# Performance work log

Measured on AMD Instinct MI355X. Metric: run time of the kernel, lower is better.

## Reference

```python
import jax, jax.numpy as jnp
import numpy as np
import math

D_MODEL = 1024
NHEAD = 16
K_DIM = D_MODEL // NHEAD
B, S = 2, 2048

def setup_inputs() -> dict:
    key = jax.random.key(0)
    ks = jax.random.split(key, 12)
    sc = 1.0 / math.sqrt(D_MODEL)
    inp = {
        'query': jax.random.normal(ks[0], (B, S, D_MODEL), jnp.float32),
        'key':   jax.random.normal(ks[1], (B, S, D_MODEL), jnp.float32),
        'value': jax.random.normal(ks[2], (B, S, D_MODEL), jnp.float32),
        'Wq': jax.random.normal(ks[3], (D_MODEL, D_MODEL), jnp.float32) * sc,
        'bq': jnp.zeros((D_MODEL,), jnp.float32),
        'Wk': jax.random.normal(ks[4], (D_MODEL, D_MODEL), jnp.float32) * sc,
        'bk': jnp.zeros((D_MODEL,), jnp.float32),
        'Wv': jax.random.normal(ks[5], (D_MODEL, D_MODEL), jnp.float32) * sc,
        'bv': jnp.zeros((D_MODEL,), jnp.float32),
        'Wo': jax.random.normal(ks[6], (D_MODEL, D_MODEL), jnp.float32) * sc,
        'bo': jnp.zeros((D_MODEL,), jnp.float32),
    }
    return inp

def reference(query, key, value, Wq, bq, Wk, bk, Wv, bv, Wo, bo):
    b, s, _ = query.shape
    # Linear projections (torch Linear: x @ W.T + b), split into heads -> [b, h, s, d]
    Q = (query @ Wq.T + bq).reshape(b, s, NHEAD, K_DIM).transpose(0, 2, 1, 3)
    K = (key   @ Wk.T + bk).reshape(b, s, NHEAD, K_DIM).transpose(0, 2, 1, 3)
    V = (value @ Wv.T + bv).reshape(b, s, NHEAD, K_DIM).transpose(0, 2, 1, 3)
    scores = jnp.einsum('bhqd,bhkd->bhqk', Q, K) / math.sqrt(K_DIM)
    attn = jax.nn.softmax(scores, axis=-1)  # dropout = identity (eval)
    out = jnp.einsum('bhqk,bhkd->bhqd', attn, V)
    out = out.transpose(0, 2, 1, 3).reshape(b, s, D_MODEL)
    out = out @ Wo.T + bo
    return (out, attn)
```

## Files before the change

kernel.cpp:

```cpp
#include <hip/hip_runtime.h>
#include <hip/hip_bf16.h>
#include <stdint.h>

#define S_LEN 2048
#define NB 2
#define NH 16
#define DM 1024
#define KDIM 64
#define MTOK (NB*S_LEN)

typedef __attribute__((ext_vector_type(8))) short bf16x8;
typedef __attribute__((ext_vector_type(4))) float f32x4;
typedef __attribute__((ext_vector_type(4))) unsigned short u16x4;
typedef __attribute__((ext_vector_type(8))) unsigned short u16x8;

#define AS1 __attribute__((address_space(1)))
#define AS3 __attribute__((address_space(3)))

__device__ __forceinline__ unsigned short f2bf(float f) {
  unsigned int u = __builtin_bit_cast(unsigned int, f);
  return (unsigned short)((u + 0x7fffu + ((u >> 16) & 1u)) >> 16);
}
__device__ __forceinline__ f32x4 mfma16(bf16x8 a, bf16x8 b, f32x4 c) {
  return __builtin_amdgcn_mfma_f32_16x16x32_bf16(a, b, c, 0, 0, 0);
}

struct CvtArgs {
  const float* src[7];
  unsigned short* dst[7];
  int n[7];
};

__global__ __launch_bounds__(256) void cvt_f32_bf16(CvtArgs a) {
  const int seg = blockIdx.y;
  const float* __restrict__ s = a.src[seg];
  unsigned short* __restrict__ d = a.dst[seg];
  const int n4 = a.n[seg] >> 2;
  const int stride = gridDim.x * blockDim.x;
  for (int i = blockIdx.x * blockDim.x + threadIdx.x; i < n4; i += stride) {
    const float4 v = reinterpret_cast<const float4*>(s)[i];
    u16x4 o;
    o[0] = f2bf(v.x); o[1] = f2bf(v.y); o[2] = f2bf(v.z); o[3] = f2bf(v.w);
    reinterpret_cast<u16x4*>(d)[i] = o;
  }
}

struct GemmArgs {
  const unsigned short* A[3];
  const unsigned short* W[3];
  const float* bias[3];
  void* dst[3];
  int mode[3];
};

__global__ __launch_bounds__(256, 2)
void gemm_pipe(GemmArgs ga)
{
  __shared__ __align__(16) char smem[32768];

  const int z = blockIdx.z;
  const unsigned short* __restrict__ A  = ga.A[z];
  const unsigned short* __restrict__ Bw = ga.W[z];
  const float* __restrict__ bias = ga.bias[z];
  void* __restrict__ dst = ga.dst[z];
  const int mode = ga.mode[z];

  const int t = threadIdx.x;
  const int w = t >> 6, l = t & 63;
  const int g = l >> 4, cl = l & 15;

  const int L   = blockIdx.x + 8 * blockIdx.y;
  const int xcd = L & 7, ix = L >> 3;
  const int m0  = (xcd * 4 + (ix & 3)) * 128;
  const int n0  = (ix >> 2) * 128;

  const unsigned short* Ag = A  + (size_t)(m0 + (t >> 2)) * DM + (t & 3) * 8;
  const unsigned short* Bg = Bw + (size_t)(n0 + (t >> 2)) * DM + (t & 3) * 8;

  const int wm = (w >> 1) * 64, wn = (w & 1) * 64;

  f32x4 acc[4][4];
  #pragma unroll
  for (int i = 0; i < 4; ++i)
    #pragma unroll
    for (int j = 0; j < 4; ++j) acc[i][j] = 0.f;

  #define STAGE(step) do {                                                          \
    AS3 char* _buf = (AS3 char*)smem + ((step) & 1) * 16384;                         \
    __builtin_amdgcn_global_load_lds((const AS1 void*)(Ag + (step)*32),              \
                                     (AS3 void*)(_buf + w*1024),          16, 0, 0); \
    __builtin_amdgcn_global_load_lds((const AS1 void*)(Ag + (step)*32 + 64*DM),      \
                                     (AS3 void*)(_buf + 4096 + w*1024),   16, 0, 0); \
    __builtin_amdgcn_global_load_lds((const AS1 void*)(Bg + (step)*32),              \
                                     (AS3 void*)(_buf + 8192 + w*1024),   16, 0, 0); \
    __builtin_amdgcn_global_load_lds((const AS1 void*)(Bg + (step)*32 + 64*DM),      \
                                     (AS3 void*)(_buf + 12288 + w*1024),  16, 0, 0); \
  } while (0)

  STAGE(0);
  for (int s = 0; s < 32; ++s) {
    if (s < 31) {
      STAGE(s + 1);
      asm volatile("s_waitcnt vmcnt(4)" ::: "memory");
    } else {
      asm volatile("s_waitcnt vmcnt(0)" ::: "memory");
    }
    __builtin_amdgcn_s_barrier();
    __builtin_amdgcn_sched_barrier(0);

    const AS3 unsigned short* bufA =
        (const AS3 unsigned short*)((AS3 char*)smem + (s & 1) * 16384);
    const AS3 unsigned short* bufB = bufA + 4096;
    bf16x8 af[4], bfv[4];
    #pragma unroll
    for (int i = 0; i < 4; ++i)
      af[i] = *(const AS3 bf16x8*)(bufA + (wm + 16*i + cl) * 32 + g*8);
    #pragma unroll
    for (int j = 0; j < 4; ++j)
      bfv[j] = *(const AS3 bf16x8*)(bufB + (wn + 16*j + cl) * 32 + g*8);
    #pragma unroll
    for (int i = 0; i < 4; ++i)
      #pragma unroll
      for (int j = 0; j < 4; ++j)
        acc[i][j] = mfma16(af[i], bfv[j], acc[i][j]);

    __builtin_amdgcn_sched_barrier(0);
    __builtin_amdgcn_s_barrier();
  }
  #undef STAGE

  if (mode == 1) {
    unsigned short* Cs = (unsigned short*)smem;
    __syncthreads();
    #pragma unroll
    for (int i = 0; i < 4; ++i) {
      #pragma unroll
      for (int j = 0; j < 4; ++j) {
        const int n = wn + 16*j + cl;
        const float bn = bias[n0 + n];
        const int u = (wm >> 2) + 4*i + g;
        const int us = u ^ (n & 31);
        u16x4 o;
        #pragma unroll
        for (int r = 0; r < 4; ++r) o[r] = f2bf(acc[i][j][r] + bn);
        *reinterpret_cast<u16x4*>(&Cs[n*128 + us*4]) = o;
      }
    }
    __syncthreads();
    {
      const int n = t >> 1, mh = (t & 1) * 64;
      const int ncol = n0 + n;
      const int h = ncol >> 6, d = ncol & (KDIM-1);
      const int b = m0 >> 11, s0 = m0 & (S_LEN-1);
      unsigned short* drow = (unsigned short*)dst
          + ((size_t)(b*NH + h)*KDIM + d)*S_LEN + s0 + mh;
      #pragma unroll
      for (int mm = 0; mm < 4; ++mm) {
        u16x4 v[4];
        #pragma unroll
        for (int k = 0; k < 4; ++k) {
          const int us = ((mh >> 2) + mm*4 + k) ^ (n & 31);
          v[k] = *reinterpret_cast<const u16x4*>(&Cs[n*128 + us*4]);
        }
        u16x8 w01, w23;
        #pragma unroll
        for (int e = 0; e < 4; ++e) {
          w01[e] = v[0][e]; w01[4+e] = v[1][e];
          w23[e] = v[2][e]; w23[4+e] = v[3][e];
        }
        *reinterpret_cast<u16x8*>(drow + mm*16)     = w01;
        *reinterpret_cast<u16x8*>(drow + mm*16 + 8) = w23;
      }
    }
  } else {
    #pragma unroll
    for (int i = 0; i < 4; ++i)
      #pragma unroll
      for (int j = 0; j < 4; ++j) {
        const int ncol = n0 + wn + 16*j + cl;
        const float bn = bias[ncol];
        #pragma unroll
        for (int r = 0; r < 4; ++r) {
          const int m = m0 + wm + 16*i + g*4 + r;
          const float v = acc[i][j][r] + bn;
          if (mode == 0) {
            const int b = m >> 11, sR = m & (S_LEN-1);
            const int h = ncol >> 6, d = ncol & (KDIM-1);
            ((unsigned short*)dst)[((size_t)(b*NH + h)*S_LEN + sR)*KDIM + d] = f2bf(v);
          } else {
            ((float*)dst)[(size_t)m * DM + ncol] = v;
          }
        }
      }
  }
}

__global__ __launch_bounds__(512, 4)
void attn_fused10(const unsigned short* __restrict__ Qh,
                  const unsigned short* __restrict__ Kh,
                  const unsigned short* __restrict__ Vt,
                  float* __restrict__ attn,
                  unsigned short* __restrict__ ctx)
{
  __shared__ __align__(16) char smem[75776];
  AS3 char* const KB = (AS3 char*)smem;
  AS3 char* const VB = (AS3 char*)smem + 32768;

  const int id  = blockIdx.x;
  const int swz = (id & 7) * 64 + (id >> 3);
  const int bh  = swz >> 4;
  const int q0  = (swz & 15) * 128;

  const int t = threadIdx.x, w = t >> 6, l = t & 63;
  const int g = l >> 4, cl = l & 15;
  AS3 char* const PBw = (AS3 char*)smem + 65536 + w * 1280;
  const int b = bh >> 4, h = bh & 15;

  const unsigned short* Qb = Qh + ((size_t)bh * S_LEN + q0 + w*16 + cl) * KDIM;
  const bf16x8 qf0 = *reinterpret_cast<const bf16x8*>(Qb + g*8);
  const bf16x8 qf1 = *reinterpret_cast<const bf16x8*>(Qb + 32 + g*8);

  const int rs = (w & 3)*8 + (l >> 3), js = l & 7;
  const unsigned short* pK = Kh + (size_t)bh*S_LEN*KDIM + (size_t)rs*KDIM
                                + (size_t)((js ^ (rs & 7)) * 8);
  const int dsv = (w & 3)*16 + (l >> 2), jv = l & 3;
  const int kst = (dsv & 3) ^ ((dsv >> 2) & 3);
  const unsigned short* pV = Vt + (size_t)bh*KDIM*S_LEN + (size_t)dsv*S_LEN
                                + (size_t)((jv ^ kst) * 8);

  const unsigned kvkey = (unsigned)((cl & 3) ^ ((cl >> 2) & 3));
  const unsigned koff0 = (unsigned)(cl*128 + ((g ^ (cl & 7)) << 4));
  const unsigned koff1 = (unsigned)(cl*128 + (((g + 4) ^ (cl & 7)) << 4));
  const float SC2 = 0.125f * 1.44269504f;

  #define STAGE_K(ch) do { int _b = (ch) & 7;                                               \
    if (w < 4) __builtin_amdgcn_global_load_lds((const AS1 void*)(pK + (size_t)(ch)*2048),  \
                   (AS3 void*)(KB + _b*4096 + (w&3)*1024), 16, 0, 0); } while (0)
  #define STAGE_KV(ch) do { int _b = (ch) & 7;                                              \
    if (w < 4) __builtin_amdgcn_global_load_lds((const AS1 void*)(pK + (size_t)(ch)*2048),  \
                   (AS3 void*)(KB + _b*4096 + (w&3)*1024), 16, 0, 0);                       \
    else       __builtin_amdgcn_global_load_lds((const AS1 void*)(pV + (size_t)(ch)*32),    \
                   (AS3 void*)(VB + _b*4096 + (w&3)*1024), 16, 0, 0); } while (0)

  float sa0 = 0.f, sa1 = 0.f, sa2 = 0.f, sa3 = 0.f;

  for (int i = 0; i < 6; ++i) STAGE_K(i);
  for (int k = 0; k < 32; ++k) {
    const int c = 2 * k;
    if (w < 4) asm volatile("s_waitcnt vmcnt(4)" ::: "memory");
    __builtin_amdgcn_s_barrier();
    __builtin_amdgcn_sched_barrier(0);
    STAGE_K(c + 6);
    STAGE_K(c + 7);
    #pragma unroll
    for (int cc = 0; cc < 2; ++cc) {
      AS3 const char* kb = KB + ((c + cc) & 7) * 4096;
      #pragma unroll
      for (int s = 0; s < 2; ++s) {
        const bf16x8 k0 = *(const AS3 bf16x8*)(kb + s*2048 + koff0);
        const bf16x8 k1 = *(const AS3 bf16x8*)(kb + s*2048 + koff1);
        f32x4 acc = {0.f, 0.f, 0.f, 0.f};
        acc = mfma16(k0, qf0, acc);
        acc = mfma16(k1, qf1, acc);
        sa0 += __builtin_exp2f(acc[0] * SC2);
        sa1 += __builtin_exp2f(acc[1] * SC2);
        sa2 += __builtin_exp2f(acc[2] * SC2);
        sa3 += __builtin_exp2f(acc[3] * SC2);
      }
    }
  }

  float ssum = (sa0 + sa1) + (sa2 + sa3);
  ssum += __shfl_xor(ssum, 16, 64);
  ssum += __shfl_xor(ssum, 32, 64);
  const float inv = 1.0f / ssum;

  __syncthreads();

  float* const arow = attn + ((size_t)bh * S_LEN + q0 + w*16 + cl) * S_LEN + g*4;
  f32x4 accP[4];
  #pragma unroll
  for (int dt = 0; dt < 4; ++dt) accP[dt] = 0.f;

  for (int i = 0; i < 6; ++i) STAGE_KV(i);
  for (int k = 0; k < 32; ++k) {
    const int c = 2 * k;
    if (k < 3) asm volatile("s_waitcnt vmcnt(4)"  ::: "memory");
    else       asm volatile("s_waitcnt vmcnt(16)" ::: "memory");
    __builtin_amdgcn_s_barrier();
    __builtin_amdgcn_sched_barrier(0);
    STAGE_KV(c + 6);
    STAGE_KV(c + 7);
    #pragma unroll
    for (int cc = 0; cc < 2; ++cc) {
      const int ch = c + cc;
      AS3 const char* kb = KB + (ch & 7) * 4096;
      AS3 const char* vb = VB + (ch & 7) * 4096;
      #pragma unroll
      for (int s = 0; s < 2; ++s) {
        const bf16x8 k0 = *(const AS3 bf16x8*)(kb + s*2048 + koff0);
        const bf16x8 k1 = *(const AS3 bf16x8*)(kb + s*2048 + koff1);
        f32x4 acc = {0.f, 0.f, 0.f, 0.f};
        acc = mfma16(k0, qf0, acc);
        acc = mfma16(k1, qf1, acc);
        f32x4 p;
        p[0] = __builtin_exp2f(acc[0] * SC2) * inv;
        p[1] = __builtin_exp2f(acc[1] * SC2) * inv;
        p[2] = __builtin_exp2f(acc[2] * SC2) * inv;
        p[3] = __builtin_exp2f(acc[3] * SC2) * inv;
        *reinterpret_cast<f32x4*>(arow + ch*32 + s*16) = p;
        u16x4 pb;
        pb[0] = f2bf(p[0]); pb[1] = f2bf(p[1]); pb[2] = f2bf(p[2]); pb[3] = f2bf(p[3]);
        *(AS3 u16x4*)(PBw + cl*80 + s*32 + g*8) = pb;
      }
      const bf16x8 ap = *(const AS3 bf16x8*)(PBw + cl*80 + g*16);
      #pragma unroll
      for (int dt = 0; dt < 4; ++dt) {
        const bf16x8 bv = *(const AS3 bf16x8*)(vb + (dt*16 + cl)*64 + ((g ^ kvkey) << 4));
        accP[dt] = mfma16(ap, bv, accP[dt]);
      }
    }
  }
  #undef STAGE_K
  #undef STAGE_KV

  #pragma unroll
  for (int r = 0; r < 4; ++r) {
    const size_t row = (size_t)(b * S_LEN + q0 + w*16 + g*4 + r);
    #pragma unroll
    for (int dt = 0; dt < 4; ++dt)
      ctx[row * DM + h * KDIM + dt*16 + cl] = f2bf(accP[dt][r]);
  }
}

extern "C" void kernel_launch(void* const* d_in, const int* in_sizes, int n_in,
                              void* d_out, int out_size, void* d_ws, size_t ws_size,
                              hipStream_t stream)
{
  const float* q_in = (const float*)d_in[0];
  const float* k_in = (const float*)d_in[1];
  const float* v_in = (const float*)d_in[2];
  const float* Wq   = (const float*)d_in[3];
  const float* bq   = (const float*)d_in[4];
  const float* Wk   = (const float*)d_in[5];
  const float* bk   = (const float*)d_in[6];
  const float* Wv   = (const float*)d_in[7];
  const float* bv   = (const float*)d_in[8];
  const float* Wo   = (const float*)d_in[9];
  const float* bo   = (const float*)d_in[10];

  unsigned short* qbf  = (unsigned short*)d_ws;
  unsigned short* kbf  = qbf  + (size_t)MTOK*DM;
  unsigned short* vbf  = kbf  + (size_t)MTOK*DM;
  unsigned short* wqbf = vbf  + (size_t)MTOK*DM;
  unsigned short* wkbf = wqbf + (size_t)DM*DM;
  unsigned short* wvbf = wkbf + (size_t)DM*DM;
  unsigned short* wobf = wvbf + (size_t)DM*DM;
  unsigned short* Qhp  = wobf + (size_t)DM*DM;
  unsigned short* Khp  = Qhp  + (size_t)MTOK*DM;
  unsigned short* Vtp  = Khp  + (size_t)MTOK*DM;
  unsigned short* ctx  = Vtp  + (size_t)MTOK*DM;

  float* out0 = (float*)d_out;
  float* attn = out0 + (size_t)MTOK*DM;

  CvtArgs ca;
  ca.src[0] = q_in; ca.dst[0] = qbf;  ca.n[0] = MTOK*DM;
  ca.src[1] = k_in; ca.dst[1] = kbf;  ca.n[1] = MTOK*DM;
  ca.src[2] = v_in; ca.dst[2] = vbf;  ca.n[2] = MTOK*DM;
  ca.src[3] = Wq;   ca.dst[3] = wqbf; ca.n[3] = DM*DM;
  ca.src[4] = Wk;   ca.dst[4] = wkbf; ca.n[4] = DM*DM;
  ca.src[5] = Wv;   ca.dst[5] = wvbf; ca.n[5] = DM*DM;
  ca.src[6] = Wo;   ca.dst[6] = wobf; ca.n[6] = DM*DM;
  cvt_f32_bf16<<<dim3(512, 7), 256, 0, stream>>>(ca);

  GemmArgs gq;
  gq.A[0] = qbf;  gq.W[0] = wqbf; gq.bias[0] = bq; gq.dst[0] = Qhp; gq.mode[0] = 0;
  gq.A[1] = kbf;  gq.W[1] = wkbf; gq.bias[1] = bk; gq.dst[1] = Khp; gq.mode[1] = 0;
  gq.A[2] = vbf;  gq.W[2] = wvbf; gq.bias[2] = bv; gq.dst[2] = Vtp; gq.mode[2] = 1;
  gemm_pipe<<<dim3(8, 32, 3), 256, 0, stream>>>(gq);

  attn_fused10<<<dim3(512), 512, 0, stream>>>(Qhp, Khp, Vtp, attn, ctx);

  GemmArgs go;
  go.A[0] = ctx; go.W[0] = wobf; go.bias[0] = bo; go.dst[0] = out0; go.mode[0] = 2;
  gemm_pipe<<<dim3(8, 32, 1), 256, 0, stream>>>(go);
}
```

Before: 268.2 us.

## Fuse activation fp32-to-bf16 conversion into QKV GEMM and deepen attention K prefetch

The QKV projection GEMM now reads fp32 activations directly, converts them to bf16 in registers and writes them into LDS, with register double-buffering two steps ahead. This removes the separate conversion pass and the bf16 activation round trip through global memory. The output projection gets its own specialized GEMM kernel. The attention first pass now keeps a 16-slot K ring buffer, with loads split across all 8 waves and 4 chunks processed per barrier. The trade-offs are more VGPR pressure in the GEMM, full vmcnt/lgkmcnt waits each step, and a larger LDS footprint in attention.

Result: no change. 273.6 us (+2.0%).

```diff
diff --git a/kernel.cpp b/kernel.cpp
--- a/kernel.cpp
+++ b/kernel.cpp
@@ -26,9 +26,9 @@
 }
 
 struct CvtArgs {
-  const float* src[7];
-  unsigned short* dst[7];
-  int n[7];
+  const float* src[4];
+  unsigned short* dst[4];
+  int n[4];
 };
 
 __global__ __launch_bounds__(256) void cvt_f32_bf16(CvtArgs a) {
@@ -45,8 +45,8 @@
   }
 }
 
-struct GemmArgs {
-  const unsigned short* A[3];
+struct GemmCvtArgs {
+  const float* A[3];
   const unsigned short* W[3];
   const float* bias[3];
   void* dst[3];
@@ -54,12 +54,12 @@
 };
 
 __global__ __launch_bounds__(256, 2)
-void gemm_pipe(GemmArgs ga)
+void gemm_cvt(GemmCvtArgs ga)
 {
   __shared__ __align__(16) char smem[32768];
 
   const int z = blockIdx.z;
-  const unsigned short* __restrict__ A  = ga.A[z];
+  const float* __restrict__ Af = ga.A[z];
   const unsigned short* __restrict__ Bw = ga.W[z];
   const float* __restrict__ bias = ga.bias[z];
   void* __restrict__ dst = ga.dst[z];
@@ -74,7 +74,7 @@
   const int m0  = (xcd * 4 + (ix & 3)) * 128;
   const int n0  = (ix >> 2) * 128;
 
-  const unsigned short* Ag = A  + (size_t)(m0 + (t >> 2)) * DM + (t & 3) * 8;
+  const float* Ap = Af + (size_t)(m0 + (t >> 2)) * DM + (t & 3) * 8;
   const unsigned short* Bg = Bw + (size_t)(n0 + (t >> 2)) * DM + (t & 3) * 8;
 
   const int wm = (w >> 1) * 64, wn = (w & 1) * 64;
@@ -85,49 +85,79 @@
     #pragma unroll
     for (int j = 0; j < 4; ++j) acc[i][j] = 0.f;
 
-  #define STAGE(step) do {                                                          \
+  #define STAGE_B(step) do {                                                        \
     AS3 char* _buf = (AS3 char*)smem + ((step) & 1) * 16384;                         \
-    __builtin_amdgcn_global_load_lds((const AS1 void*)(Ag + (step)*32),              \
-                                     (AS3 void*)(_buf + w*1024),          16, 0, 0); \
-    __builtin_amdgcn_global_load_lds((const AS1 void*)(Ag + (step)*32 + 64*DM),      \
-                                     (AS3 void*)(_buf + 4096 + w*1024),   16, 0, 0); \
     __builtin_amdgcn_global_load_lds((const AS1 void*)(Bg + (step)*32),              \
                                      (AS3 void*)(_buf + 8192 + w*1024),   16, 0, 0); \
     __builtin_amdgcn_global_load_lds((const AS1 void*)(Bg + (step)*32 + 64*DM),      \
                                      (AS3 void*)(_buf + 12288 + w*1024),  16, 0, 0); \
   } while (0)
 
-  STAGE(0);
-  for (int s = 0; s < 32; ++s) {
-    if (s < 31) {
-      STAGE(s + 1);
-      asm volatile("s_waitcnt vmcnt(4)" ::: "memory");
-    } else {
-      asm volatile("s_waitcnt vmcnt(0)" ::: "memory");
-    }
-    __builtin_amdgcn_s_barrier();
-    __builtin_amdgcn_sched_barrier(0);
-
-    const AS3 unsigned short* bufA =
-        (const AS3 unsigned short*)((AS3 char*)smem + (s & 1) * 16384);
-    const AS3 unsigned short* bufB = bufA + 4096;
-    bf16x8 af[4], bfv[4];
-    #pragma unroll
-    for (int i = 0; i < 4; ++i)
-      af[i] = *(const AS3 bf16x8*)(bufA + (wm + 16*i + cl) * 32 + g*8);
-    #pragma unroll
-    for (int j = 0; j < 4; ++j)
-      bfv[j] = *(const AS3 bf16x8*)(bufB + (wn + 16*j + cl) * 32 + g*8);
-    #pragma unroll
-    for (int i = 0; i < 4; ++i)
-      #pragma unroll
-      for (int j = 0; j < 4; ++j)
-        acc[i][j] = mfma16(af[i], bfv[j], acc[i][j]);
-
-    __builtin_amdgcn_sched_barrier(0);
-    __builtin_amdgcn_s_barrier();
-  }
-  #undef STAGE
+  #define ALOAD(step, ra, rb, rc, rd) do {                                           \
+    const float* _p = Ap + (step) * 32;                                              \
+    ra = *reinterpret_cast<const float4*>(_p);                                       \
+    rb = *reinterpret_cast<const float4*>(_p + 4);                                   \
+    const float* _q = _p + (size_t)64 * DM;                                          \
+    rc = *reinterpret_cast<const float4*>(_q);                                       \
+    rd = *reinterpret_cast<const float4*>(_q + 4);                                   \
+  } while (0)
+
+  #define AWRITE(step, ra, rb, rc, rd) do {                                          \
+    AS3 char* _buf = (AS3 char*)smem + ((step) & 1) * 16384;                         \
+    u16x8 _w0, _w1;                                                                  \
+    _w0[0]=f2bf(ra.x); _w0[1]=f2bf(ra.y); _w0[2]=f2bf(ra.z); _w0[3]=f2bf(ra.w);      \
+    _w0[4]=f2bf(rb.x); _w0[5]=f2bf(rb.y); _w0[6]=f2bf(rb.z); _w0[7]=f2bf(rb.w);      \
+    _w1[0]=f2bf(rc.x); _w1[1]=f2bf(rc.y); _w1[2]=f2bf(rc.z); _w1[3]=f2bf(rc.w);      \
+    _w1[4]=f2bf(rd.x); _w1[5]=f2bf(rd.y); _w1[6]=f2bf(rd.z); _w1[7]=f2bf(rd.w);      \
+    *(AS3 u16x8*)(_buf + t*16) = _w0;                                                \
+    *(AS3 u16x8*)(_buf + 4096 + t*16) = _w1;                                         \
+  } while (0)
+
+  #define COMPUTE(s) do {                                                            \
+    const AS3 unsigned short* bufA =                                                 \
+        (const AS3 unsigned short*)((AS3 char*)smem + ((s) & 1) * 16384);            \
+    const AS3 unsigned short* bufB = bufA + 4096;                                    \
+    bf16x8 af[4], bfv[4];                                                            \
+    _Pragma("unroll")                                                                \
+    for (int i = 0; i < 4; ++i)                                                      \
+      af[i] = *(const AS3 bf16x8*)(bufA + (wm + 16*i + cl) * 32 + g*8);              \
+    _Pragma("unroll")                                                                \
+    for (int j = 0; j < 4; ++j)                                                      \
+      bfv[j] = *(const AS3 bf16x8*)(bufB + (wn + 16*j + cl) * 32 + g*8);             \
+    _Pragma("unroll")                                                                \
+    for (int i = 0; i < 4; ++i)                                                      \
+      _Pragma("unroll")                                                              \
+      for (int j = 0; j < 4; ++j)                                                    \
+        acc[i][j] = mfma16(af[i], bfv[j], acc[i][j]);                                \
+  } while (0)
+
+  #define GSEC(s, c0,c1,c2,c3, n0_,n1_,n2_,n3_) do {                                 \
+    asm volatile("s_waitcnt vmcnt(0)" ::: "memory");                                 \
+    asm volatile("s_waitcnt lgkmcnt(0)" ::: "memory");                               \
+    __builtin_amdgcn_s_barrier();                                                    \
+    __builtin_amdgcn_sched_barrier(0);                                               \
+    if ((s) + 1 < 32) STAGE_B((s) + 1);                                              \
+    if ((s) + 2 < 32) ALOAD((s) + 2, n0_, n1_, n2_, n3_);                            \
+    if ((s) + 1 < 32) AWRITE((s) + 1, c0, c1, c2, c3);                               \
+    COMPUTE(s);                                                                      \
+  } while (0)
+
+  float4 e0, e1, e2, e3, o0, o1, o2, o3;
+  STAGE_B(0);
+  ALOAD(0, e0, e1, e2, e3);
+  ALOAD(1, o0, o1, o2, o3);
+  asm volatile("s_waitcnt vmcnt(4)" ::: "memory");
+  AWRITE(0, e0, e1, e2, e3);
+
+  for (int sp = 0; sp < 16; ++sp) {
+    GSEC(2*sp,     o0, o1, o2, o3,  e0, e1, e2, e3);
+    GSEC(2*sp + 1, e0, e1, e2, e3,  o0, o1, o2, o3);
+  }
+  #undef GSEC
+  #undef COMPUTE
+  #undef AWRITE
+  #undef ALOAD
+  #undef STAGE_B
 
   if (mode == 1) {
     unsigned short* Cs = (unsigned short*)smem;
@@ -183,20 +213,102 @@
         for (int r = 0; r < 4; ++r) {
           const int m = m0 + wm + 16*i + g*4 + r;
           const float v = acc[i][j][r] + bn;
-          if (mode == 0) {
-            const int b = m >> 11, sR = m & (S_LEN-1);
-            const int h = ncol >> 6, d = ncol & (KDIM-1);
-            ((unsigned short*)dst)[((size_t)(b*NH + h)*S_LEN + sR)*KDIM + d] = f2bf(v);
-          } else {
-            ((float*)dst)[(size_t)m * DM + ncol] = v;
-          }
+          const int b = m >> 11, sR = m & (S_LEN-1);
+          const int h = ncol >> 6, d = ncol & (KDIM-1);
+          ((unsigned short*)dst)[((size_t)(b*NH + h)*S_LEN + sR)*KDIM + d] = f2bf(v);
         }
       }
   }
 }
 
+__global__ __launch_bounds__(256, 2)
+void gemm_pipe(const unsigned short* __restrict__ A,
+               const unsigned short* __restrict__ Bw,
+               const float* __restrict__ bias,
+               float* __restrict__ dst)
+{
+  __shared__ __align__(16) char smem[32768];
+
+  const int t = threadIdx.x;
+  const int w = t >> 6, l = t & 63;
+  const int g = l >> 4, cl = l & 15;
+
+  const int L   = blockIdx.x + 8 * blockIdx.y;
+  const int xcd = L & 7, ix = L >> 3;
+  const int m0  = (xcd * 4 + (ix & 3)) * 128;
+  const int n0  = (ix >> 2) * 128;
+
+  const unsigned short* Ag = A  + (size_t)(m0 + (t >> 2)) * DM + (t & 3) * 8;
+  const unsigned short* Bg = Bw + (size_t)(n0 + (t >> 2)) * DM + (t & 3) * 8;
+
+  const int wm = (w >> 1) * 64, wn = (w & 1) * 64;
+
+  f32x4 acc[4][4];
+  #pragma unroll
+  for (int i = 0; i < 4; ++i)
+    #pragma unroll
+    for (int j = 0; j < 4; ++j) acc[i][j] = 0.f;
+
+  #define STAGE(step) do {                                                          \
+    AS3 char* _buf = (AS3 char*)smem + ((step) & 1) * 16384;                         \
+    __builtin_amdgcn_global_load_lds((const AS1 void*)(Ag + (step)*32),              \
+                                     (AS3 void*)(_buf + w*1024),          16, 0, 0); \
+    __builtin_amdgcn_global_load_lds((const AS1 void*)(Ag + (step)*32 + 64*DM),      \
+                                     (AS3 void*)(_buf + 4096 + w*1024),   16, 0, 0); \
+    __builtin_amdgcn_global_load_lds((const AS1 void*)(Bg + (step)*32),              \
+                                     (AS3 void*)(_buf + 8192 + w*1024),   16, 0, 0); \
+    __builtin_amdgcn_global_load_lds((const AS1 void*)(Bg + (step)*32 + 64*DM),      \
+                                     (AS3 void*)(_buf + 12288 + w*1024),  16, 0, 0); \
+  } while (0)
+
+  STAGE(0);
+  for (int s = 0; s < 32; ++s) {
+    if (s < 31) {
+      STAGE(s + 1);
+      asm volatile("s_waitcnt vmcnt(4)" ::: "memory");
+    } else {
+      asm volatile("s_waitcnt vmcnt(0)" ::: "memory");
+    }
+    __builtin_amdgcn_s_barrier();
+    __builtin_amdgcn_sched_barrier(0);
+
+    const AS3 unsigned short* bufA =
+        (const AS3 unsigned short*)((AS3 char*)smem + (s & 1) * 16384);
+    const AS3 unsigned short* bufB = bufA + 4096;
+    bf16x8 af[4], bfv[4];
+    #pragma unroll
+    for (int i = 0; i < 4; ++i)
+      af[i] = *(const AS3 bf16x8*)(bufA + (wm + 16*i + cl) * 32 + g*8);
+    #pragma unroll
+    for (int j = 0; j < 4; ++j)
+      bfv[j] = *(const AS3 bf16x8*)(bufB + (wn + 16*j + cl) * 32 + g*8);
+    #pragma unroll
+    for (int i = 0; i < 4; ++i)
+      #pragma unroll
+      for (int j = 0; j < 4; ++j)
+        acc[i][j] = mfma16(af[i], bfv[j], acc[i][j]);
+
+    __builtin_amdgcn_sched_barrier(0);
+    __builtin_amdgcn_s_barrier();
+  }
+  #undef STAGE
+
+  #pragma unroll
+  for (int i = 0; i < 4; ++i)
+    #pragma unroll
+    for (int j = 0; j < 4; ++j) {
+      const int ncol = n0 + wn + 16*j + cl;
+      const float bn = bias[ncol];
+      #pragma unroll
+      for (int r = 0; r < 4; ++r) {
+        const int m = m0 + wm + 16*i + g*4 + r;
+        dst[(size_t)m * DM + ncol] = acc[i][j][r] + bn;
+      }
+    }
+}
+
 __global__ __launch_bounds__(512, 4)
-void attn_fused10(const unsigned short* __restrict__ Qh,
+void attn_fused11(const unsigned short* __restrict__ Qh,
                   const unsigned short* __restrict__ Kh,
                   const unsigned short* __restrict__ Vt,
                   float* __restrict__ attn,
@@ -233,9 +345,9 @@
   const unsigned koff1 = (unsigned)(cl*128 + (((g + 4) ^ (cl & 7)) << 4));
   const float SC2 = 0.125f * 1.44269504f;
 
-  #define STAGE_K(ch) do { int _b = (ch) & 7;                                               \
-    if (w < 4) __builtin_amdgcn_global_load_lds((const AS1 void*)(pK + (size_t)(ch)*2048),  \
-                   (AS3 void*)(KB + _b*4096 + (w&3)*1024), 16, 0, 0); } while (0)
+  #define STAGE_A(ch) do { if (((ch) < 64) && (((ch) & 1) == (w >> 2)))             \
+      __builtin_amdgcn_global_load_lds((const AS1 void*)(pK + (size_t)(ch)*2048),   \
+          (AS3 void*)(KB + ((ch) & 15)*4096 + (w & 3)*1024), 16, 0, 0); } while (0)
   #define STAGE_KV(ch) do { int _b = (ch) & 7;                                              \
     if (w < 4) __builtin_amdgcn_global_load_lds((const AS1 void*)(pK + (size_t)(ch)*2048),  \
                    (AS3 void*)(KB + _b*4096 + (w&3)*1024), 16, 0, 0);                       \
@@ -244,17 +356,16 @@
 
   float sa0 = 0.f, sa1 = 0.f, sa2 = 0.f, sa3 = 0.f;
 
-  for (int i = 0; i < 6; ++i) STAGE_K(i);
-  for (int k = 0; k < 32; ++k) {
-    const int c = 2 * k;
-    if (w < 4) asm volatile("s_waitcnt vmcnt(4)" ::: "memory");
+  for (int i = 0; i < 8; ++i) STAGE_A(i);
+  for (int k = 0; k < 16; ++k) {
+    const int c = 4 * k;
+    asm volatile("s_waitcnt vmcnt(2)" ::: "memory");
     __builtin_amdgcn_s_barrier();
     __builtin_amdgcn_sched_barrier(0);
-    STAGE_K(c + 6);
-    STAGE_K(c + 7);
-    #pragma unroll
-    for (int cc = 0; cc < 2; ++cc) {
-      AS3 const char* kb = KB + ((c + cc) & 7) * 4096;
+    STAGE_A(c + 8); STAGE_A(c + 9); STAGE_A(c + 10); STAGE_A(c + 11);
+    #pragma unroll
+    for (int cc = 0; cc < 4; ++cc) {
+      AS3 const char* kb = KB + ((c + cc) & 15) * 4096;
       #pragma unroll
       for (int s = 0; s < 2; ++s) {
         const bf16x8 k0 = *(const AS3 bf16x8*)(kb + s*2048 + koff0);
@@ -321,7 +432,7 @@
       }
     }
   }
-  #undef STAGE_K
+  #undef STAGE_A
   #undef STAGE_KV
 
   #pragma unroll
@@ -349,10 +460,7 @@
   const float* Wo   = (const float*)d_in[9];
   const float* bo   = (const float*)d_in[10];
 
-  unsigned short* qbf  = (unsigned short*)d_ws;
-  unsigned short* kbf  = qbf  + (size_t)MTOK*DM;
-  unsigned short* vbf  = kbf  + (size_t)MTOK*DM;
-  unsigned short* wqbf = vbf  + (size_t)MTOK*DM;
+  unsigned short* wqbf = (unsigned short*)d_ws;
   unsigned short* wkbf = wqbf + (size_t)DM*DM;
   unsigned short* wvbf = wkbf + (size_t)DM*DM;
   unsigned short* wobf = wvbf + (size_t)DM*DM;
@@ -365,24 +473,19 @@
   float* attn = out0 + (size_t)MTOK*DM;
 
   CvtArgs ca;
-  ca.src[0] = q_in; ca.dst[0] = qbf;  ca.n[0] = MTOK*DM;
-  ca.src[1] = k_in; ca.dst[1] = kbf;  ca.n[1] = MTOK*DM;
-  ca.src[2] = v_in; ca.dst[2] = vbf;  ca.n[2] = MTOK*DM;
-  ca.src[3] = Wq;   ca.dst[3] = wqbf; ca.n[3] = DM*DM;
-  ca.src[4] = Wk;   ca.dst[4] = wkbf; ca.n[4] = DM*DM;
-  ca.src[5] = Wv;   ca.dst[5] = wvbf; ca.n[5] = DM*DM;
-  ca.src[6] = Wo;   ca.dst[6] = wobf; ca.n[6] = DM*DM;
-  cvt_f32_bf16<<<dim3(512, 7), 256, 0, stream>>>(ca);
-
-  GemmArgs gq;
-  gq.A[0] = qbf;  gq.W[0] = wqbf; gq.bias[0] = bq; gq.dst[0] = Qhp; gq.mode[0] = 0;
-  gq.A[1] = kbf;  gq.W[1] = wkbf; gq.bias[1] = bk; gq.dst[1] = Khp; gq.mode[1] = 0;
-  gq.A[2] = vbf;  gq.W[2] = wvbf; gq.bias[2] = bv; gq.dst[2] = Vtp; gq.mode[2] = 1;
-  gemm_pipe<<<dim3(8, 32, 3), 256, 0, stream>>>(gq);
-
-  attn_fused10<<<dim3(512), 512, 0, stream>>>(Qhp, Khp, Vtp, attn, ctx);
-
-  GemmArgs go;
-  go.A[0] = ctx; go.W[0] = wobf; go.bias[0] = bo; go.dst[0] = out0; go.mode[0] = 2;
-  gemm_pipe<<<dim3(8, 32, 1), 256, 0, stream>>>(go);
-}
+  ca.src[0] = Wq; ca.dst[0] = wqbf; ca.n[0] = DM*DM;
+  ca.src[1] = Wk; ca.dst[1] = wkbf; ca.n[1] = DM*DM;
+  ca.src[2] = Wv; ca.dst[2] = wvbf; ca.n[2] = DM*DM;
+  ca.src[3] = Wo; ca.dst[3] = wobf; ca.n[3] = DM*DM;
+  cvt_f32_bf16<<<dim3(64, 4), 256, 0, stream>>>(ca);
+
+  GemmCvtArgs gq;
+  gq.A[0] = q_in; gq.W[0] = wqbf; gq.bias[0] = bq; gq.dst[0] = Qhp; gq.mode[0] = 0;
+  gq.A[1] = k_in; gq.W[1] = wkbf; gq.bias[1] = bk; gq.dst[1] = Khp; gq.mode[1] = 0;
+  gq.A[2] = v_in; gq.W[2] = wvbf; gq.bias[2] = bv; gq.dst[2] = Vtp; gq.mode[2] = 1;
+  gemm_cvt<<<dim3(8, 32, 3), 256, 0, stream>>>(gq);
+
+  attn_fused11<<<dim3(512), 512, 0, stream>>>(Qhp, Khp, Vtp, attn, ctx);
+
+  gemm_pipe<<<dim3(8, 32), 256, 0, stream>>>(ctx, wobf, bo, out0);
+}
```
